# Performance work log

Measured on AMD Instinct MI355X. Metric: run time of the kernel, lower is better.

The kernel has to match this reference:

```python
import jax, jax.numpy as jnp
import numpy as np

B, N, D, NUM_K = 128, 1024, 64, 8


def setup_inputs() -> dict:
    key = jax.random.key(0)
    k1, k2, k3 = jax.random.split(key, 3)
    nodes = jax.random.normal(k1, (B, N, D), dtype=jnp.float32)
    # xavier_uniform over (in_dims, in_dims) fan: bound = sqrt(6 / (N + N))
    bound = float(np.sqrt(6.0 / (N + N)))
    weight = jax.random.uniform(k2, (NUM_K, N, N), dtype=jnp.float32,
                                minval=-bound, maxval=bound)
    graph_shift = jax.random.normal(k3, (N, N), dtype=jnp.float32) / np.sqrt(N)
    return {"nodes": nodes, "weight": weight, "graph_shift": graph_shift}


def reference(nodes, weight, graph_shift):
    """Polynomial graph filter: out[b] = sum_k W_k @ S^k @ X_b.

    Since sum_k W_k S^k X = (sum_k W_k S^k) X, we fuse all taps into one
    N x N operator A, then apply a single batched GEMM over the batch.
    """
    n = nodes.shape[1]
    eye = jnp.eye(n, dtype=nodes.dtype)

    def step(S, Wk):
        # emit W_k @ S^k, carry S^{k+1}
        return S @ graph_shift, Wk @ S

    _, Mk = jax.lax.scan(step, eye, weight)   # [num_k, N, N]
    A = Mk.sum(axis=0)                        # fused filter operator [N, N]
    return jnp.einsum('nm,bmd->bnd', A, nodes)  # [B, N, D]
```

## Files before the change

kernel.cpp:

```cpp
#include <hip/hip_runtime.h>
#include <stdint.h>


#define NN 1024
#define NBATCH 128
#define DDIM 64

typedef float floatx4 __attribute__((ext_vector_type(4)));
typedef _Float16 f16x8 __attribute__((ext_vector_type(8)));
typedef unsigned short u16;

__device__ __forceinline__ u16 f2h(float f) {
  union { _Float16 h; u16 u; } v; v.h = (_Float16)f; return v.u;
}
__device__ __forceinline__ float h2f(u16 u) {
  union { _Float16 h; u16 u; } v; v.u = u; return (float)v.h;
}

__device__ __forceinline__ void gll16(const void* g, void* l) {
  __builtin_amdgcn_global_load_lds(
      (const __attribute__((address_space(1))) void*)g,
      (__attribute__((address_space(3))) void*)l, 16, 0, 0);
}

template <int ROWS>
__device__ __forceinline__ void stage64(const u16* __restrict__ g, u16* lds,
                                        int wave, int lane) {
  const int r = lane >> 3, c = lane & 7;
  const int sw = (c ^ r) * 8;
#pragma unroll
  for (int i = 0; i < ROWS / 32; ++i) {
    const int rb = wave * (ROWS / 4) + i * 8;
    gll16(g + (size_t)(rb + r) * NN + sw, lds + rb * 64);
  }
}

struct CvtJob { const float* src; u16* rm; u16* cm; };
struct CvtJobs { CvtJob j[5]; };

__global__ __launch_bounds__(256) void cvt_kernel(CvtJobs jobs) {
  CvtJob jb = jobs.j[blockIdx.z];
  int idx4 = blockIdx.x * 256 + threadIdx.x;
  int e = idx4 * 4;
  int row = e >> 10, col = e & (NN - 1);
  float4 f = ((const float4*)jb.src)[idx4];
  u16 h[4] = { f2h(f.x), f2h(f.y), f2h(f.z), f2h(f.w) };
  uint2 p;
  p.x = (uint32_t)h[0] | ((uint32_t)h[1] << 16);
  p.y = (uint32_t)h[2] | ((uint32_t)h[3] << 16);
  *(uint2*)&jb.rm[e] = p;
  if (jb.cm) {
#pragma unroll
    for (int i = 0; i < 4; ++i) jb.cm[(size_t)(col + i) * NN + row] = h[i];
  }
}

__global__ __launch_bounds__(256) void transpose_x(const float* __restrict__ X,
                                                   u16* __restrict__ XT) {
  __shared__ u16 T[64][72];
  const int k0 = blockIdx.x * 64;
  const int b = blockIdx.y;
  const int t = threadIdx.x;
#pragma unroll
  for (int it = 0; it < 4; ++it) {
    int kr = (t >> 4) + it * 16;
    int d4 = (t & 15) * 4;
    float4 f = *(const float4*)&X[((size_t)b * NN + k0 + kr) * DDIM + d4];
    T[d4 + 0][kr] = f2h(f.x);
    T[d4 + 1][kr] = f2h(f.y);
    T[d4 + 2][kr] = f2h(f.z);
    T[d4 + 3][kr] = f2h(f.w);
  }
  __syncthreads();
#pragma unroll
  for (int it = 0; it < 2; ++it) {
    int d = (t >> 3) + it * 32;
    int kc = (t & 7) * 8;
    *(uint4*)&XT[((size_t)b * DDIM + d) * NN + k0 + kc] = *(uint4*)&T[d][kc];
  }
}

struct GemmJob {
  const u16* A;
  const u16* B;
  const float* addF;
  const u16* addH;
  u16* outRm;
  u16* outCm;
  float* outP;
};
struct GemmJobs { GemmJob j[5]; };

template <int BM, int BN, int KSPLIT>
__global__ __launch_bounds__(256) void gemm_f16(GemmJobs jobs) {
  const GemmJob jb = jobs.j[blockIdx.z / KSPLIT];
  const int chunk = blockIdx.z % KSPLIT;
  __shared__ u16 As[BM * 64], Bs[BN * 64];
  const int t = threadIdx.x, wave = t >> 6, lane = t & 63;
  const int wm = wave >> 1, wn = wave & 1;
  const int lm = lane & 15, q = lane >> 4;
  const int bm = blockIdx.x * BM, bn = blockIdx.y * BN;
  constexpr int MI = BM / 32, NI = BN / 32, KTPB = 16 / KSPLIT;
  floatx4 acc[MI][NI] = {};

  for (int kk = 0; kk < KTPB; ++kk) {
    const int kt = chunk * KTPB + kk;
    __syncthreads();
    stage64<BM>(jb.A + (size_t)bm * NN + kt * 64, As, wave, lane);
    stage64<BN>(jb.B + (size_t)bn * NN + kt * 64, Bs, wave, lane);
    __syncthreads();
#pragma unroll
    for (int ks = 0; ks < 2; ++ks) {
      const int st = ((ks * 4 + q) ^ (lm & 7)) * 8;
      f16x8 bf[NI];
#pragma unroll
      for (int ni = 0; ni < NI; ++ni)
        bf[ni] = *(const f16x8*)&Bs[(wn * (BN / 2) + ni * 16 + lm) * 64 + st];
#pragma unroll
      for (int mi = 0; mi < MI; ++mi) {
        f16x8 a = *(const f16x8*)&As[(wm * (BM / 2) + mi * 16 + lm) * 64 + st];
#pragma unroll
        for (int ni = 0; ni < NI; ++ni)
          acc[mi][ni] = __builtin_amdgcn_mfma_f32_16x16x32_f16(a, bf[ni], acc[mi][ni], 0, 0, 0);
      }
    }
  }

  if (KSPLIT > 1) {
    float* p = jb.outP + (size_t)chunk * NN * NN;
#pragma unroll
    for (int mi = 0; mi < MI; ++mi)
#pragma unroll
      for (int ni = 0; ni < NI; ++ni)
#pragma unroll
        for (int r = 0; r < 4; ++r) {
          int row = bm + wm * (BM / 2) + mi * 16 + q * 4 + r;
          int col = bn + wn * (BN / 2) + ni * 16 + lm;
          p[(size_t)row * NN + col] = acc[mi][ni][r];
        }
  } else {
#pragma unroll
    for (int mi = 0; mi < MI; ++mi)
#pragma unroll
      for (int ni = 0; ni < NI; ++ni)
#pragma unroll
        for (int r = 0; r < 4; ++r) {
          int row = bm + wm * (BM / 2) + mi * 16 + q * 4 + r;
          int col = bn + wn * (BN / 2) + ni * 16 + lm;
          size_t rm = (size_t)row * NN + col;
          float v = acc[mi][ni][r];
          if (jb.addF) v += jb.addF[rm];
          if (jb.addH) v += h2f(jb.addH[rm]);
          u16 h = f2h(v);
          if (jb.outRm) jb.outRm[rm] = h;
          if (jb.outCm) jb.outCm[(size_t)col * NN + row] = h;
        }
  }
}

__global__ __launch_bounds__(256) void combine_A(const float* __restrict__ parts,
                                                 const u16* __restrict__ v0,
                                                 u16* __restrict__ A) {
  int e = (blockIdx.x * 256 + threadIdx.x) * 4;
  float4 s = *(const float4*)&parts[e];
#pragma unroll
  for (int z = 1; z < 4; ++z) {
    float4 p = *(const float4*)&parts[(size_t)z * NN * NN + e];
    s.x += p.x; s.y += p.y; s.z += p.z; s.w += p.w;
  }
  uint2 h = *(const uint2*)&v0[e];
  uint2 o;
  o.x = (uint32_t)f2h(s.x + h2f((u16)h.x)) |
        ((uint32_t)f2h(s.y + h2f((u16)(h.x >> 16))) << 16);
  o.y = (uint32_t)f2h(s.z + h2f((u16)h.y)) |
        ((uint32_t)f2h(s.w + h2f((u16)(h.y >> 16))) << 16);
  *(uint2*)&A[e] = o;
}

__global__ __launch_bounds__(256) void apply_gemm(const u16* __restrict__ A,
                                                  const u16* __restrict__ XT,
                                                  float* __restrict__ out) {
  __shared__ u16 As[8192], Xs[4096];
  const int t = threadIdx.x, wave = t >> 6, lane = t & 63;
  const int lm = lane & 15, q = lane >> 4;
  const int b = blockIdx.x, bm = blockIdx.y * 128;
  floatx4 acc[2][4] = {};

  for (int kt = 0; kt < 16; ++kt) {
    __syncthreads();
    stage64<128>(A + (size_t)bm * NN + kt * 64, As, wave, lane);
    stage64<64>(XT + (size_t)b * DDIM * NN + kt * 64, Xs, wave, lane);
    __syncthreads();
#pragma unroll
    for (int ks = 0; ks < 2; ++ks) {
      const int st = ((ks * 4 + q) ^ (lm & 7)) * 8;
      f16x8 x[4];
#pragma unroll
      for (int ni = 0; ni < 4; ++ni)
        x[ni] = *(const f16x8*)&Xs[(ni * 16 + lm) * 64 + st];
#pragma unroll
      for (int mi = 0; mi < 2; ++mi) {
        f16x8 a = *(const f16x8*)&As[(wave * 32 + mi * 16 + lm) * 64 + st];
#pragma unroll
        for (int ni = 0; ni < 4; ++ni)
          acc[mi][ni] = __builtin_amdgcn_mfma_f32_16x16x32_f16(a, x[ni], acc[mi][ni], 0, 0, 0);
      }
    }
  }

#pragma unroll
  for (int mi = 0; mi < 2; ++mi)
#pragma unroll
    for (int ni = 0; ni < 4; ++ni)
#pragma unroll
      for (int r = 0; r < 4; ++r) {
        int row = bm + wave * 32 + mi * 16 + q * 4 + r;
        int d = ni * 16 + lm;
        out[((size_t)b * NN + row) * DDIM + d] = acc[mi][ni][r];
      }
}

extern "C" void kernel_launch(void* const* d_in, const int* in_sizes, int n_in,
                              void* d_out, int out_size, void* d_ws, size_t ws_size,
                              hipStream_t stream) {
  const float* nodes  = (const float*)d_in[0];
  const float* weight = (const float*)d_in[1];
  const float* gs     = (const float*)d_in[2];
  float* out = (float*)d_out;
  u16* ws = (u16*)d_ws;
  const size_t MB = (size_t)NN * NN;
  auto buf = [&](int i) -> u16* { return ws + (size_t)i * MB; };

  CvtJobs cv{};
  cv.j[0] = { gs,              buf(0), buf(1) };
  cv.j[1] = { weight + 1 * MB, buf(2), nullptr };
  cv.j[2] = { weight + 3 * MB, buf(3), nullptr };
  cv.j[3] = { weight + 5 * MB, buf(4), nullptr };
  cv.j[4] = { weight + 7 * MB, buf(5), nullptr };
  cvt_kernel<<<dim3(NN * NN / 1024, 1, 5), 256, 0, stream>>>(cv);

  GemmJobs g1{};
  g1.j[0] = { buf(0), buf(1), nullptr,         nullptr, buf(6),  buf(7),  nullptr };
  g1.j[1] = { buf(2), buf(1), weight + 0 * MB, nullptr, buf(8),  nullptr, nullptr };
  g1.j[2] = { buf(3), buf(1), weight + 2 * MB, nullptr, buf(9),  nullptr, nullptr };
  g1.j[3] = { buf(4), buf(1), weight + 4 * MB, nullptr, buf(10), nullptr, nullptr };
  g1.j[4] = { buf(5), buf(1), weight + 6 * MB, nullptr, buf(11), nullptr, nullptr };
  gemm_f16<64, 128, 1><<<dim3(16, 8, 5), 256, 0, stream>>>(g1);

  u16* XT = buf(16);
  transpose_x<<<dim3(16, NBATCH), 256, 0, stream>>>(nodes, XT);

  GemmJobs g2{};
  g2.j[0] = { buf(6),  buf(7), nullptr, nullptr, nullptr, buf(12), nullptr };
  g2.j[1] = { buf(9),  buf(7), nullptr, buf(8),  buf(13), nullptr, nullptr };
  g2.j[2] = { buf(11), buf(7), nullptr, buf(10), buf(14), nullptr, nullptr };
  gemm_f16<64, 64, 1><<<dim3(16, 16, 3), 256, 0, stream>>>(g2);

  float* parts = (float*)buf(24);
  GemmJobs g3{};
  g3.j[0] = { buf(14), buf(12), nullptr, nullptr, nullptr, nullptr, parts };
  gemm_f16<64, 64, 4><<<dim3(16, 16, 4), 256, 0, stream>>>(g3);

  combine_A<<<dim3(NN * NN / 1024), 256, 0, stream>>>(parts, buf(13), buf(15));

  apply_gemm<<<dim3(NBATCH, 8), 256, 0, stream>>>(buf(15), XT, out);
}
```

Measured before the change: 201.7 us.

## Double-buffer LDS in GEMMs, enlarge tiles, and merge batches in apply GEMM

Adds LDS double buffering to the generic f16 GEMM and the apply GEMM, so the next K-tile is staged while MFMAs run on the current one, with one barrier per iteration. Tile shapes grow to 128x128 for several launches via new wave-layout template parameters. The apply GEMM now treats two batches' X^T as one 128-wide N tile, which raises per-block reuse of A. The trade-off is double the LDS per block and fewer blocks (e.g. 320 or 256 per launch), which may reduce occupancy and wave-level parallelism on a 256-CU part.

Measured after the change: 220.5 us. 9.3% more time.

```diff
diff --git a/kernel.cpp b/kernel.cpp
--- a/kernel.cpp
+++ b/kernel.cpp
@@ -91,42 +91,51 @@
 };
 struct GemmJobs { GemmJob j[5]; };
 
-template <int BM, int BN, int KSPLIT>
+template <int BM, int BN, int WM, int WN, int KSPLIT>
 __global__ __launch_bounds__(256) void gemm_f16(GemmJobs jobs) {
   const GemmJob jb = jobs.j[blockIdx.z / KSPLIT];
   const int chunk = blockIdx.z % KSPLIT;
-  __shared__ u16 As[BM * 64], Bs[BN * 64];
+  __shared__ u16 As[2][BM * 64], Bs[2][BN * 64];
   const int t = threadIdx.x, wave = t >> 6, lane = t & 63;
-  const int wm = wave >> 1, wn = wave & 1;
+  const int wm = wave / WN, wn = wave % WN;
   const int lm = lane & 15, q = lane >> 4;
   const int bm = blockIdx.x * BM, bn = blockIdx.y * BN;
-  constexpr int MI = BM / 32, NI = BN / 32, KTPB = 16 / KSPLIT;
+  constexpr int MI = BM / (WM * 16), NI = BN / (WN * 16);
+  constexpr int KTPB = 16 / KSPLIT;
   floatx4 acc[MI][NI] = {};
 
+  const u16* Ag = jb.A + (size_t)bm * NN + chunk * KTPB * 64;
+  const u16* Bg = jb.B + (size_t)bn * NN + chunk * KTPB * 64;
+
+  stage64<BM>(Ag, As[0], wave, lane);
+  stage64<BN>(Bg, Bs[0], wave, lane);
+  __syncthreads();
+
   for (int kk = 0; kk < KTPB; ++kk) {
-    const int kt = chunk * KTPB + kk;
-    __syncthreads();
-    stage64<BM>(jb.A + (size_t)bm * NN + kt * 64, As, wave, lane);
-    stage64<BN>(jb.B + (size_t)bn * NN + kt * 64, Bs, wave, lane);
-    __syncthreads();
+    const int cur = kk & 1;
+    if (kk + 1 < KTPB) {
+      stage64<BM>(Ag + (kk + 1) * 64, As[cur ^ 1], wave, lane);
+      stage64<BN>(Bg + (kk + 1) * 64, Bs[cur ^ 1], wave, lane);
+    }
 #pragma unroll
     for (int ks = 0; ks < 2; ++ks) {
       const int st = ((ks * 4 + q) ^ (lm & 7)) * 8;
       f16x8 bf[NI];
 #pragma unroll
       for (int ni = 0; ni < NI; ++ni)
-        bf[ni] = *(const f16x8*)&Bs[(wn * (BN / 2) + ni * 16 + lm) * 64 + st];
+        bf[ni] = *(const f16x8*)&Bs[cur][(wn * (BN / WN) + ni * 16 + lm) * 64 + st];
 #pragma unroll
       for (int mi = 0; mi < MI; ++mi) {
-        f16x8 a = *(const f16x8*)&As[(wm * (BM / 2) + mi * 16 + lm) * 64 + st];
+        f16x8 a = *(const f16x8*)&As[cur][(wm * (BM / WM) + mi * 16 + lm) * 64 + st];
 #pragma unroll
         for (int ni = 0; ni < NI; ++ni)
           acc[mi][ni] = __builtin_amdgcn_mfma_f32_16x16x32_f16(a, bf[ni], acc[mi][ni], 0, 0, 0);
       }
     }
-  }
-
-  if (KSPLIT > 1) {
+    __syncthreads();
+  }
+
+  if constexpr (KSPLIT > 1) {
     float* p = jb.outP + (size_t)chunk * NN * NN;
 #pragma unroll
     for (int mi = 0; mi < MI; ++mi)
@@ -134,8 +143,8 @@
       for (int ni = 0; ni < NI; ++ni)
 #pragma unroll
         for (int r = 0; r < 4; ++r) {
-          int row = bm + wm * (BM / 2) + mi * 16 + q * 4 + r;
-          int col = bn + wn * (BN / 2) + ni * 16 + lm;
+          int row = bm + wm * (BM / WM) + mi * 16 + q * 4 + r;
+          int col = bn + wn * (BN / WN) + ni * 16 + lm;
           p[(size_t)row * NN + col] = acc[mi][ni][r];
         }
   } else {
@@ -145,8 +154,8 @@
       for (int ni = 0; ni < NI; ++ni)
 #pragma unroll
         for (int r = 0; r < 4; ++r) {
-          int row = bm + wm * (BM / 2) + mi * 16 + q * 4 + r;
-          int col = bn + wn * (BN / 2) + ni * 16 + lm;
+          int row = bm + wm * (BM / WM) + mi * 16 + q * 4 + r;
+          int col = bn + wn * (BN / WN) + ni * 16 + lm;
           size_t rm = (size_t)row * NN + col;
           float v = acc[mi][ni][r];
           if (jb.addF) v += jb.addF[rm];
@@ -180,43 +189,54 @@
 __global__ __launch_bounds__(256) void apply_gemm(const u16* __restrict__ A,
                                                   const u16* __restrict__ XT,
                                                   float* __restrict__ out) {
-  __shared__ u16 As[8192], Xs[4096];
+  __shared__ u16 As[2][128 * 64], Xs[2][128 * 64];
   const int t = threadIdx.x, wave = t >> 6, lane = t & 63;
+  const int wm = wave >> 1, wn = wave & 1;
   const int lm = lane & 15, q = lane >> 4;
-  const int b = blockIdx.x, bm = blockIdx.y * 128;
-  floatx4 acc[2][4] = {};
+  const int bn = blockIdx.x * 128;
+  const int bm = blockIdx.y * 128;
+  floatx4 acc[4][4] = {};
+  const u16* Ag = A + (size_t)bm * NN;
+  const u16* Xg = XT + (size_t)bn * NN;
+
+  stage64<128>(Ag, As[0], wave, lane);
+  stage64<128>(Xg, Xs[0], wave, lane);
+  __syncthreads();
 
   for (int kt = 0; kt < 16; ++kt) {
-    __syncthreads();
-    stage64<128>(A + (size_t)bm * NN + kt * 64, As, wave, lane);
-    stage64<64>(XT + (size_t)b * DDIM * NN + kt * 64, Xs, wave, lane);
-    __syncthreads();
+    const int cur = kt & 1;
+    if (kt + 1 < 16) {
+      stage64<128>(Ag + (kt + 1) * 64, As[cur ^ 1], wave, lane);
+      stage64<128>(Xg + (kt + 1) * 64, Xs[cur ^ 1], wave, lane);
+    }
 #pragma unroll
     for (int ks = 0; ks < 2; ++ks) {
       const int st = ((ks * 4 + q) ^ (lm & 7)) * 8;
-      f16x8 x[4];
+      f16x8 xf[4];
 #pragma unroll
       for (int ni = 0; ni < 4; ++ni)
-        x[ni] = *(const f16x8*)&Xs[(ni * 16 + lm) * 64 + st];
-#pragma unroll
-      for (int mi = 0; mi < 2; ++mi) {
-        f16x8 a = *(const f16x8*)&As[(wave * 32 + mi * 16 + lm) * 64 + st];
+        xf[ni] = *(const f16x8*)&Xs[cur][(wn * 64 + ni * 16 + lm) * 64 + st];
+#pragma unroll
+      for (int mi = 0; mi < 4; ++mi) {
+        f16x8 a = *(const f16x8*)&As[cur][(wm * 64 + mi * 16 + lm) * 64 + st];
 #pragma unroll
         for (int ni = 0; ni < 4; ++ni)
-          acc[mi][ni] = __builtin_amdgcn_mfma_f32_16x16x32_f16(a, x[ni], acc[mi][ni], 0, 0, 0);
+          acc[mi][ni] = __builtin_amdgcn_mfma_f32_16x16x32_f16(a, xf[ni], acc[mi][ni], 0, 0, 0);
       }
     }
-  }
-
-#pragma unroll
-  for (int mi = 0; mi < 2; ++mi)
+    __syncthreads();
+  }
+
+#pragma unroll
+  for (int mi = 0; mi < 4; ++mi)
 #pragma unroll
     for (int ni = 0; ni < 4; ++ni)
 #pragma unroll
       for (int r = 0; r < 4; ++r) {
-        int row = bm + wave * 32 + mi * 16 + q * 4 + r;
-        int d = ni * 16 + lm;
-        out[((size_t)b * NN + row) * DDIM + d] = acc[mi][ni][r];
+        int row = bm + wm * 64 + mi * 16 + q * 4 + r;
+        int col = bn + wn * 64 + ni * 16 + lm;
+        out[((size_t)(col >> 6) * NN + row) * DDIM + (col & 63)] =
+            acc[mi][ni][r];
       }
 }
 
@@ -245,7 +265,7 @@
   g1.j[2] = { buf(3), buf(1), weight + 2 * MB, nullptr, buf(9),  nullptr, nullptr };
   g1.j[3] = { buf(4), buf(1), weight + 4 * MB, nullptr, buf(10), nullptr, nullptr };
   g1.j[4] = { buf(5), buf(1), weight + 6 * MB, nullptr, buf(11), nullptr, nullptr };
-  gemm_f16<64, 128, 1><<<dim3(16, 8, 5), 256, 0, stream>>>(g1);
+  gemm_f16<128, 128, 2, 2, 1><<<dim3(8, 8, 5), 256, 0, stream>>>(g1);
 
   u16* XT = buf(16);
   transpose_x<<<dim3(16, NBATCH), 256, 0, stream>>>(nodes, XT);
@@ -254,14 +274,14 @@
   g2.j[0] = { buf(6),  buf(7), nullptr, nullptr, nullptr, buf(12), nullptr };
   g2.j[1] = { buf(9),  buf(7), nullptr, buf(8),  buf(13), nullptr, nullptr };
   g2.j[2] = { buf(11), buf(7), nullptr, buf(10), buf(14), nullptr, nullptr };
-  gemm_f16<64, 64, 1><<<dim3(16, 16, 3), 256, 0, stream>>>(g2);
+  gemm_f16<64, 128, 2, 2, 1><<<dim3(16, 8, 3), 256, 0, stream>>>(g2);
 
   float* parts = (float*)buf(24);
   GemmJobs g3{};
   g3.j[0] = { buf(14), buf(12), nullptr, nullptr, nullptr, nullptr, parts };
-  gemm_f16<64, 64, 4><<<dim3(16, 16, 4), 256, 0, stream>>>(g3);
+  gemm_f16<128, 128, 2, 2, 4><<<dim3(8, 8, 4), 256, 0, stream>>>(g3);
 
   combine_A<<<dim3(NN * NN / 1024), 256, 0, stream>>>(parts, buf(13), buf(15));
 
-  apply_gemm<<<dim3(NBATCH, 8), 256, 0, stream>>>(buf(15), XT, out);
-}
+  apply_gemm<<<dim3(64, 8), 256, 0, stream>>>(buf(15), XT, out);
+}
```
